# Kernel optimization log

Measured on AMD Instinct MI355X. Metric: run time of the kernel, lower is better.

The kernel has to match this reference:

```python
import jax, jax.numpy as jnp
import numpy as np

N, E = 50000, 800000
HID, HEADS, EDIM = 64, 4, 32
HC = HID * HEADS
NEG_SLOPE = 0.2
LN_EPS = 1e-5


def setup_inputs() -> dict:
    key = jax.random.key(0)
    ks = jax.random.split(key, 16)
    s = lambda d: 1.0 / np.sqrt(d)
    return {
        "x": jax.random.normal(ks[0], (N, HID), jnp.float32),
        "edge_index": jax.random.randint(ks[1], (2, E), 0, N, jnp.int64),
        "edge_attr": jax.random.normal(ks[2], (E, EDIM), jnp.float32),
        # GATv2Conv params
        "W_l": jax.random.normal(ks[3], (HID, HC), jnp.float32) * s(HID),
        "b_l": jnp.zeros((HC,), jnp.float32),
        "W_r": jax.random.normal(ks[4], (HID, HC), jnp.float32) * s(HID),
        "b_r": jnp.zeros((HC,), jnp.float32),
        "W_e": jax.random.normal(ks[5], (EDIM, HC), jnp.float32) * s(EDIM),
        "att": jax.random.normal(ks[6], (HEADS, HID), jnp.float32) * s(HID),
        "bias_gat": jnp.zeros((HC,), jnp.float32),
        # block params
        "W1": jax.random.normal(ks[7], (HID, HC), jnp.float32) * s(HID),
        "b1": jnp.zeros((HC,), jnp.float32),
        "gamma": jnp.ones((HC,), jnp.float32),
        "beta": jnp.zeros((HC,), jnp.float32),
        "W2": jax.random.normal(ks[8], (HC, HID), jnp.float32) * s(HC),
        "b2": jnp.zeros((HID,), jnp.float32),
    }


def _gatv2(x, edge_index, edge_attr, W_l, b_l, W_r, b_r, W_e, att, bias_gat):
    src, dst = edge_index[0], edge_index[1]
    x_l = (x @ W_l + b_l).reshape(N, HEADS, HID)  # source transform
    x_r = (x @ W_r + b_r).reshape(N, HEADS, HID)  # target transform
    e = (edge_attr @ W_e).reshape(E, HEADS, HID)
    m = x_l[src] + x_r[dst] + e                    # [E, H, C]
    m = jax.nn.leaky_relu(m, NEG_SLOPE)
    alpha = jnp.einsum('ehc,hc->eh', m, att)       # [E, H]
    # segment softmax over incoming edges of each target node
    amax = jax.ops.segment_max(alpha, dst, num_segments=N)
    alpha = jnp.exp(alpha - amax[dst])
    denom = jax.ops.segment_sum(alpha, dst, num_segments=N)
    alpha = alpha / (denom[dst] + 1e-16)
    out = jax.ops.segment_sum(x_l[src] * alpha[..., None], dst, num_segments=N)
    return out.reshape(N, HC) + bias_gat


def reference(x, edge_index, edge_attr, W_l, b_l, W_r, b_r, W_e, att, bias_gat,
              W1, b1, gamma, beta, W2, b2):
    h = _gatv2(x, edge_index, edge_attr, W_l, b_l, W_r, b_r, W_e, att, bias_gat)
    xl = jnp.tanh(x @ W1 + b1)
    z = xl + h
    mu = jnp.mean(z, axis=-1, keepdims=True)
    var = jnp.var(z, axis=-1, keepdims=True)
    z = (z - mu) * jax.lax.rsqrt(var + LN_EPS) * gamma + beta
    return jnp.tanh(z @ W2 + b2)
```

## Files before the change

kernel.cpp:

```cpp
#include <hip/hip_runtime.h>
#include <math.h>

#define N_NODES 50000
#define N_EDGES 800000
#define HID 64
#define HEADS 4
#define HC 256
#define NEG_SLOPE 0.2f
#define LN_EPS 1e-5f
#define EDGE_BLOCKS 2048

typedef __attribute__((ext_vector_type(8))) short bf16x8;
typedef __attribute__((ext_vector_type(8))) unsigned short u16x8;
typedef __attribute__((ext_vector_type(4))) float f32x4;

__device__ __forceinline__ float bf2f(unsigned short u) {
    return __uint_as_float(((unsigned int)u) << 16);
}
__device__ __forceinline__ unsigned short f2bf(float f) {
    unsigned int u = __float_as_uint(f);
    u = (u + 0x7fffu + ((u >> 16) & 1u)) >> 16;
    return (unsigned short)u;
}
__device__ __forceinline__ float fast_tanh(float v) {
    const float c = fminf(fmaxf(v, -15.f), 15.f);
    const float e = __expf(2.f * c);
    return 1.f - 2.f / (e + 1.f);
}
__device__ __forceinline__ bf16x8 pack_bf8(float4 a, float4 b) {
    u16x8 r;
    r[0] = f2bf(a.x); r[1] = f2bf(a.y); r[2] = f2bf(a.z); r[3] = f2bf(a.w);
    r[4] = f2bf(b.x); r[5] = f2bf(b.y); r[6] = f2bf(b.z); r[7] = f2bf(b.w);
    return __builtin_bit_cast(bf16x8, r);
}

__global__ __launch_bounds__(256) void k_ntm(
    const float* __restrict__ x,
    const float* __restrict__ W_l, const float* __restrict__ b_l,
    const float* __restrict__ W_r, const float* __restrict__ b_r,
    unsigned short* __restrict__ xl_t, unsigned short* __restrict__ xr_t)
{
    __shared__ unsigned short wl_s[2][16][64][8];
    __shared__ unsigned short wr_s[2][16][64][8];
    const int t = threadIdx.x, lane = t & 63, wv = t >> 6;
    const int arow = lane & 15, koct = lane >> 4;

    for (int i = t; i < 2048; i += 256) {
        const int ks = i >> 10, nt = (i >> 6) & 15, ls = i & 63;
        const int col = nt * 16 + (ls & 15);
        const int kb = ks * 32 + (ls >> 4) * 8;
        unsigned short a[8], b[8];
#pragma unroll
        for (int j = 0; j < 8; j++) {
            a[j] = f2bf(W_l[(kb + j) * 256 + col]);
            b[j] = f2bf(W_r[(kb + j) * 256 + col]);
        }
        *(ushort4*)&wl_s[ks][nt][ls][0] = make_ushort4(a[0], a[1], a[2], a[3]);
        *(ushort4*)&wl_s[ks][nt][ls][4] = make_ushort4(a[4], a[5], a[6], a[7]);
        *(ushort4*)&wr_s[ks][nt][ls][0] = make_ushort4(b[0], b[1], b[2], b[3]);
        *(ushort4*)&wr_s[ks][nt][ls][4] = make_ushort4(b[4], b[5], b[6], b[7]);
    }
    __syncthreads();

    const int n0w = blockIdx.x * 64 + wv * 16;
    if (n0w >= N_NODES) return;

    const float* xrow = x + (size_t)(n0w + arow) * 64;
    const bf16x8 af0 = pack_bf8(*(const float4*)(xrow + koct * 8),
                                *(const float4*)(xrow + koct * 8 + 4));
    const bf16x8 af1 = pack_bf8(*(const float4*)(xrow + 32 + koct * 8),
                                *(const float4*)(xrow + 32 + koct * 8 + 4));

    float acc[4][16];
#pragma unroll
    for (int nt = 0; nt < 16; nt++) {
        const float bv = b_l[nt * 16 + arow];
        f32x4 d = {bv, bv, bv, bv};
        d = __builtin_amdgcn_mfma_f32_16x16x32_bf16(af0, *(const bf16x8*)&wl_s[0][nt][lane][0], d, 0, 0, 0);
        d = __builtin_amdgcn_mfma_f32_16x16x32_bf16(af1, *(const bf16x8*)&wl_s[1][nt][lane][0], d, 0, 0, 0);
#pragma unroll
        for (int r = 0; r < 4; r++) acc[r][nt] = d[r];
    }
#pragma unroll
    for (int r = 0; r < 4; r++) {
        u16x8 lo, hi;
#pragma unroll
        for (int j = 0; j < 8; j++) { lo[j] = f2bf(acc[r][j]); hi[j] = f2bf(acc[r][j + 8]); }
        unsigned short* dst = xl_t + (size_t)(n0w + koct * 4 + r) * 256 + arow * 16;
        *(u16x8*)dst = lo;
        *(u16x8*)(dst + 8) = hi;
    }
#pragma unroll
    for (int nt = 0; nt < 16; nt++) {
        const float bv = b_r[nt * 16 + arow];
        f32x4 d = {bv, bv, bv, bv};
        d = __builtin_amdgcn_mfma_f32_16x16x32_bf16(af0, *(const bf16x8*)&wr_s[0][nt][lane][0], d, 0, 0, 0);
        d = __builtin_amdgcn_mfma_f32_16x16x32_bf16(af1, *(const bf16x8*)&wr_s[1][nt][lane][0], d, 0, 0, 0);
#pragma unroll
        for (int r = 0; r < 4; r++) acc[r][nt] = d[r];
    }
#pragma unroll
    for (int r = 0; r < 4; r++) {
        u16x8 lo, hi;
#pragma unroll
        for (int j = 0; j < 8; j++) { lo[j] = f2bf(acc[r][j]); hi[j] = f2bf(acc[r][j + 8]); }
        unsigned short* dst = xr_t + (size_t)(n0w + koct * 4 + r) * 256 + arow * 16;
        *(u16x8*)dst = lo;
        *(u16x8*)(dst + 8) = hi;
    }
}

__global__ __launch_bounds__(256) void k_permw(
    const float* __restrict__ W1, const float* __restrict__ b1,
    const float* __restrict__ gamma, const float* __restrict__ beta,
    const float* __restrict__ bias_gat, const float* __restrict__ W2,
    float* __restrict__ W1p, float* __restrict__ b1p,
    float* __restrict__ gammap, float* __restrict__ betap,
    float* __restrict__ biasgp, float* __restrict__ W2p)
{
    const int c = threadIdx.x;
    const int pos = (c & 15) * 16 + (c >> 4);
    for (int k = 0; k < 64; k++) W1p[k * 256 + pos] = W1[k * 256 + c];
    b1p[pos] = b1[c];
    gammap[pos] = gamma[c];
    betap[pos] = beta[c];
    biasgp[pos] = bias_gat[c];
    for (int j = 0; j < 64; j++) W2p[pos * 64 + j] = W2[c * 64 + j];
}

__global__ __launch_bounds__(256) void k_hist(const int* __restrict__ ei, int* __restrict__ count)
{
    const int e = blockIdx.x * 256 + threadIdx.x;
    if (e < N_EDGES) atomicAdd(&count[ei[N_EDGES + e]], 1);
}

__global__ __launch_bounds__(1024) void k_scan(const int* __restrict__ count, int* __restrict__ off)
{
    __shared__ int wsum[16];
    __shared__ int s_carry;
    const int t = threadIdx.x, lane = t & 63, wv = t >> 6;
    if (t == 0) s_carry = 0;
    __syncthreads();
    for (int base = 0; base < N_NODES; base += 8192) {
        const int idx0 = base + t * 8;
        int v[8];
#pragma unroll
        for (int j = 0; j < 8; j++) { int i = idx0 + j; v[j] = (i < N_NODES) ? count[i] : 0; }
#pragma unroll
        for (int j = 1; j < 8; j++) v[j] += v[j - 1];
        const int tot = v[7];
        int sc = tot;
#pragma unroll
        for (int s = 1; s < 64; s <<= 1) { int o = __shfl_up(sc, s, 64); if (lane >= s) sc += o; }
        if (lane == 63) wsum[wv] = sc;
        __syncthreads();
        const int carry = s_carry;
        int woff = 0;
        for (int u = 0; u < wv; u++) woff += wsum[u];
        const int ebase = carry + woff + (sc - tot);
#pragma unroll
        for (int j = 0; j < 8; j++) {
            int i = idx0 + j;
            if (i < N_NODES) off[i] = ebase + (j ? v[j - 1] : 0);
        }
        __syncthreads();
        if (t == 0) { int tt = 0; for (int u = 0; u < 16; u++) tt += wsum[u]; s_carry = carry + tt; }
        __syncthreads();
    }
    if (threadIdx.x == 0) off[N_NODES] = s_carry;
}

__global__ __launch_bounds__(256) void k_scatter(
    const int* __restrict__ ei, const int* __restrict__ off, int* __restrict__ cursor,
    int* __restrict__ csr_src, int* __restrict__ eid_csr)
{
    const int e = blockIdx.x * 256 + threadIdx.x;
    if (e < N_EDGES) {
        const int s = ei[e];
        const int d = ei[N_EDGES + e];
        const int pos = off[d] + atomicAdd(&cursor[d], 1);
        csr_src[pos] = s;
        eid_csr[pos] = e;
    }
}

template<bool F32>
__global__ __launch_bounds__(256) void k_edgeagg(
    const int* __restrict__ off, const int* __restrict__ csr_src,
    const int* __restrict__ eid_csr, const float* __restrict__ edge_attr,
    const float* __restrict__ W_e, const float* __restrict__ att,
    const unsigned short* __restrict__ xl_t, const unsigned short* __restrict__ xr_t,
    void* __restrict__ zs_g)
{
    __shared__ unsigned short bfrag_s[16][64][8];

    const int t = threadIdx.x;
    const int lane = t & 63, wv = t >> 6;
    const int arow = lane & 15, koct = lane >> 4;

    for (int i = t; i < 1024; i += 256) {
        const int nt = i >> 6, ls = i & 63;
        const int col = nt * 16 + (ls & 15);
        const int kb = (ls >> 4) * 8;
        unsigned short tmp[8];
#pragma unroll
        for (int j = 0; j < 8; j++) tmp[j] = f2bf(W_e[(kb + j) * 256 + col]);
        *(ushort4*)&bfrag_s[nt][ls][0] = make_ushort4(tmp[0], tmp[1], tmp[2], tmp[3]);
        *(ushort4*)&bfrag_s[nt][ls][4] = make_ushort4(tmp[4], tmp[5], tmp[6], tmp[7]);
    }
    __syncthreads();

    float attLf[8], attHf[8];
#pragma unroll
    for (int j = 0; j < 8; j++) {
        attLf[j] = att[j * 16 + arow];
        attHf[j] = att[(j + 8) * 16 + arow];
    }

    const int STRIDE = EDGE_BLOCKS * 4;
    int node = blockIdx.x * 4 + wv;
    if (node >= N_NODES) return;

    int lo = off[node], hi = off[node + 1];
    u16x8 xrl = *(const u16x8*)(xr_t + (size_t)node * 256 + arow * 16);
    u16x8 xrh = *(const u16x8*)(xr_t + (size_t)node * 256 + arow * 16 + 8);
    while (hi <= lo) {
        if (F32) *(float4*)((float*)zs_g + (size_t)node * 256 + arow * 16 + koct * 4) = make_float4(0.f, 0.f, 0.f, 0.f);
        else *(ushort4*)((unsigned short*)zs_g + (size_t)node * 256 + arow * 16 + koct * 4) = make_ushort4(0, 0, 0, 0);
        node += STRIDE;
        if (node >= N_NODES) return;
        lo = off[node]; hi = off[node + 1];
        xrl = *(const u16x8*)(xr_t + (size_t)node * 256 + arow * 16);
        xrh = *(const u16x8*)(xr_t + (size_t)node * 256 + arow * 16 + 8);
    }
    int svbase = lo;
    int svall = csr_src[min(svbase + lane, hi - 1)];
    int evall = eid_csr[min(svbase + lane, hi - 1)];

    int nnode = node + STRIDE;
    bool nvalid = nnode < N_NODES;
    int nlo = 0, nhi = 0, nsvall = 0, nevall = 0;
    u16x8 nxrl = xrl, nxrh = xrh;
    if (nvalid) {
        nlo = off[nnode]; nhi = off[nnode + 1];
        nxrl = *(const u16x8*)(xr_t + (size_t)nnode * 256 + arow * 16);
        nxrh = *(const u16x8*)(xr_t + (size_t)nnode * 256 + arow * 16 + 8);
        if (nhi > nlo) {
            nsvall = csr_src[min(nlo + lane, nhi - 1)];
            nevall = eid_csr[min(nlo + lane, nhi - 1)];
        }
    }
    int p0 = lo;
    bf16x8 af;
    u16x8 xlo[4], xhi[4];
    {
        const int eid0 = __shfl(evall, arow, 64);
        const float* ap = edge_attr + (size_t)eid0 * 32 + koct * 8;
        af = pack_bf8(*(const float4*)ap, *(const float4*)(ap + 4));
#pragma unroll
        for (int r = 0; r < 4; r++) {
            const int sr = __shfl(svall, koct * 4 + r, 64);
            const unsigned short* bp = xl_t + (size_t)sr * 256 + arow * 16;
            xlo[r] = *(const u16x8*)bp;
            xhi[r] = *(const u16x8*)(bp + 8);
        }
    }

    float g[16];
#pragma unroll
    for (int i = 0; i < 16; i++) g[i] = 0.f;
    float dsum[4] = {0.f, 0.f, 0.f, 0.f};

    for (;;) {
        const bool last = (p0 + 16 >= hi);
        bool uvalid;
        int up0;
        if (!last) { uvalid = true; up0 = p0 + 16; }
        else {
            while (nvalid && nlo >= nhi) {
                if (F32) *(float4*)((float*)zs_g + (size_t)nnode * 256 + arow * 16 + koct * 4) = make_float4(0.f, 0.f, 0.f, 0.f);
                else *(ushort4*)((unsigned short*)zs_g + (size_t)nnode * 256 + arow * 16 + koct * 4) = make_ushort4(0, 0, 0, 0);
                nnode += STRIDE;
                nvalid = nnode < N_NODES;
                if (nvalid) {
                    nlo = off[nnode]; nhi = off[nnode + 1];
                    nxrl = *(const u16x8*)(xr_t + (size_t)nnode * 256 + arow * 16);
                    nxrh = *(const u16x8*)(xr_t + (size_t)nnode * 256 + arow * 16 + 8);
                    if (nhi > nlo) {
                        nsvall = csr_src[min(nlo + lane, nhi - 1)];
                        nevall = eid_csr[min(nlo + lane, nhi - 1)];
                    }
                }
            }
            uvalid = nvalid; up0 = nlo;
        }
        float4 uA0 = make_float4(0.f, 0.f, 0.f, 0.f), uA1 = uA0;
        if (uvalid) {
            const int ubase = last ? 0 : (up0 - svbase);
            const int uev = last ? nevall : evall;
            const int ueid = __shfl(uev, ubase + arow, 64);
            const float* ap = edge_attr + (size_t)ueid * 32 + koct * 8;
            uA0 = *(const float4*)ap;
            uA1 = *(const float4*)(ap + 4);
        }

        float s_[4][4];
#pragma unroll
        for (int r = 0; r < 4; r++)
#pragma unroll
            for (int h = 0; h < 4; h++) s_[r][h] = 0.f;

#pragma unroll
        for (int nt = 0; nt < 8; nt++) {
            const bf16x8 bfr = *(const bf16x8*)&bfrag_s[nt][lane][0];
            const float xrv = bf2f((unsigned short)xrl[nt]);
            f32x4 dacc = {xrv, xrv, xrv, xrv};
            dacc = __builtin_amdgcn_mfma_f32_16x16x32_bf16(af, bfr, dacc, 0, 0, 0);
            const float atv = attLf[nt];
            const int h = nt >> 2;
#pragma unroll
            for (int r = 0; r < 4; r++) {
                const float mm = dacc[r] + bf2f((unsigned short)xlo[r][nt]);
                const float lk = fmaxf(mm, NEG_SLOPE * mm);
                s_[r][h] = fmaf(atv, lk, s_[r][h]);
            }
        }
        u16x8 uxlo[4], uxhi[4];
        if (uvalid) {
            const int ubase = last ? 0 : (up0 - svbase);
            const int usrcv = last ? nsvall : svall;
#pragma unroll
            for (int r = 0; r < 4; r++) {
                const int sr = __shfl(usrcv, ubase + koct * 4 + r, 64);
                const unsigned short* bp = xl_t + (size_t)sr * 256 + arow * 16;
                uxlo[r] = *(const u16x8*)bp;
                uxhi[r] = *(const u16x8*)(bp + 8);
            }
        } else {
#pragma unroll
            for (int r = 0; r < 4; r++) { uxlo[r] = xlo[r]; uxhi[r] = xhi[r]; }
        }
#pragma unroll
        for (int n2 = 0; n2 < 8; n2++) {
            const int nt = n2 + 8;
            const bf16x8 bfr = *(const bf16x8*)&bfrag_s[nt][lane][0];
            const float xrv = bf2f((unsigned short)xrh[n2]);
            f32x4 dacc = {xrv, xrv, xrv, xrv};
            dacc = __builtin_amdgcn_mfma_f32_16x16x32_bf16(af, bfr, dacc, 0, 0, 0);
            const float atv = attHf[n2];
            const int h = nt >> 2;
#pragma unroll
            for (int r = 0; r < 4; r++) {
                const float mm = dacc[r] + bf2f((unsigned short)xhi[r][n2]);
                const float lk = fmaxf(mm, NEG_SLOPE * mm);
                s_[r][h] = fmaf(atv, lk, s_[r][h]);
            }
        }
#pragma unroll
        for (int r = 0; r < 4; r++)
#pragma unroll
            for (int h = 0; h < 4; h++) {
                float v = s_[r][h];
                v += __shfl_xor(v, 1, 64);
                v += __shfl_xor(v, 2, 64);
                v += __shfl_xor(v, 4, 64);
                v += __shfl_xor(v, 8, 64);
                s_[r][h] = v;
            }
#pragma unroll
        for (int h = 0; h < 4; h++) {
            float w4[4];
#pragma unroll
            for (int r = 0; r < 4; r++) {
                const bool ok = (p0 + koct * 4 + r) < hi;
                w4[r] = ok ? __expf(fminf(s_[r][h], 60.f)) : 0.f;
            }
            dsum[h] += (w4[0] + w4[1]) + (w4[2] + w4[3]);
#pragma unroll
            for (int q = 0; q < 4; q++) {
                const int nt = h * 4 + q;
                float acc = g[nt];
#pragma unroll
                for (int r = 0; r < 4; r++) {
                    const float xv = bf2f((unsigned short)(nt < 8 ? xlo[r][nt & 7] : xhi[r][nt & 7]));
                    acc = fmaf(w4[r], xv, acc);
                }
                g[nt] = acc;
            }
        }

        if (last) {
#pragma unroll
            for (int i = 0; i < 16; i++) {
                float v = g[i];
                v += __shfl_xor(v, 16, 64);
                v += __shfl_xor(v, 32, 64);
                g[i] = v;
            }
#pragma unroll
            for (int h = 0; h < 4; h++) {
                float v = dsum[h];
                v += __shfl_xor(v, 16, 64);
                v += __shfl_xor(v, 32, 64);
                dsum[h] = v;
            }
            const float inv = 1.f / (dsum[koct] + 1e-16f);
            if (F32) {
                *(float4*)((float*)zs_g + (size_t)node * 256 + arow * 16 + koct * 4) =
                    make_float4(g[koct * 4] * inv, g[koct * 4 + 1] * inv,
                                g[koct * 4 + 2] * inv, g[koct * 4 + 3] * inv);
            } else {
                *(ushort4*)((unsigned short*)zs_g + (size_t)node * 256 + arow * 16 + koct * 4) =
                    make_ushort4(f2bf(g[koct * 4] * inv), f2bf(g[koct * 4 + 1] * inv),
                                 f2bf(g[koct * 4 + 2] * inv), f2bf(g[koct * 4 + 3] * inv));
            }
            if (!uvalid) return;
            node = nnode; lo = nlo; hi = nhi; xrl = nxrl; xrh = nxrh;
            svbase = nlo; svall = nsvall; evall = nevall;
#pragma unroll
            for (int i = 0; i < 16; i++) g[i] = 0.f;
#pragma unroll
            for (int h = 0; h < 4; h++) dsum[h] = 0.f;
            nnode += STRIDE;
            nvalid = nnode < N_NODES;
            if (nvalid) {
                nlo = off[nnode]; nhi = off[nnode + 1];
                nxrl = *(const u16x8*)(xr_t + (size_t)nnode * 256 + arow * 16);
                nxrh = *(const u16x8*)(xr_t + (size_t)nnode * 256 + arow * 16 + 8);
                if (nhi > nlo) {
                    nsvall = csr_src[min(nlo + lane, nhi - 1)];
                    nevall = eid_csr[min(nlo + lane, nhi - 1)];
                }
            }
        }
        p0 = up0;
        af = pack_bf8(uA0, uA1);
#pragma unroll
        for (int r = 0; r < 4; r++) { xlo[r] = uxlo[r]; xhi[r] = uxhi[r]; }
        if (p0 - svbase >= 32) {
            svbase = p0;
            svall = csr_src[min(svbase + lane, hi - 1)];
            evall = eid_csr[min(svbase + lane, hi - 1)];
        }
    }
}

template<bool F32>
__global__ __launch_bounds__(256) void k_post(
    const void* __restrict__ zs_g, const float* __restrict__ x,
    const float* __restrict__ biasgp,
    const float* __restrict__ W1p, const float* __restrict__ b1p,
    const float* __restrict__ gammap, const float* __restrict__ betap,
    const float* __restrict__ W2p, const float* __restrict__ b2,
    float* __restrict__ out)
{
    __shared__ unsigned short wf[16384];
    __shared__ unsigned short zsh[64][272];
    __shared__ float outsh[64][64];

    const int t = threadIdx.x, lane = t & 63, wv = t >> 6;
    const int arow = lane & 15, koct = lane >> 4;
    const int n0 = blockIdx.x * 64;
    const int nw = n0 + wv * 16;

    for (int i = t; i < 2048; i += 256) {
        const int ks = i >> 10, nt = (i >> 6) & 15, ls = i & 63;
        const int col = (ls & 15) * 16 + nt;
        const int kb = ks * 32 + (ls >> 4) * 8;
        unsigned short a[8];
#pragma unroll
        for (int j = 0; j < 8; j++) a[j] = f2bf(W1p[(kb + j) * 256 + col]);
        *(ushort4*)&wf[i * 8]     = make_ushort4(a[0], a[1], a[2], a[3]);
        *(ushort4*)&wf[i * 8 + 4] = make_ushort4(a[4], a[5], a[6], a[7]);
    }
    __syncthreads();

    const int xn = min(nw + arow, N_NODES - 1);
    const float* xrow = x + (size_t)xn * 64;
    const bf16x8 af0 = pack_bf8(*(const float4*)(xrow + koct * 8),
                                *(const float4*)(xrow + koct * 8 + 4));
    const bf16x8 af1 = pack_bf8(*(const float4*)(xrow + 32 + koct * 8),
                                *(const float4*)(xrow + 32 + koct * 8 + 4));

    float z[4][16];
#pragma unroll
    for (int nt = 0; nt < 16; nt++) {
        const float bv = b1p[arow * 16 + nt];
        f32x4 d = {bv, bv, bv, bv};
        d = __builtin_amdgcn_mfma_f32_16x16x32_bf16(af0, *(const bf16x8*)&wf[(0 * 16 + nt) * 512 + lane * 8], d, 0, 0, 0);
        d = __builtin_amdgcn_mfma_f32_16x16x32_bf16(af1, *(const bf16x8*)&wf[(1 * 16 + nt) * 512 + lane * 8], d, 0, 0, 0);
#pragma unroll
        for (int r = 0; r < 4; r++) z[r][nt] = d[r];
    }
#pragma unroll
    for (int r = 0; r < 4; r++) {
        const int nd = min(nw + koct * 4 + r, N_NODES - 1);
        float gv[16];
        if (F32) {
            const float* gp = (const float*)zs_g + (size_t)nd * 256 + arow * 16;
#pragma unroll
            for (int i4 = 0; i4 < 4; i4++) {
                const float4 v = *(const float4*)(gp + i4 * 4);
                gv[i4 * 4] = v.x; gv[i4 * 4 + 1] = v.y; gv[i4 * 4 + 2] = v.z; gv[i4 * 4 + 3] = v.w;
            }
        } else {
            const unsigned short* gp = (const unsigned short*)zs_g + (size_t)nd * 256 + arow * 16;
            const u16x8 a = *(const u16x8*)gp;
            const u16x8 b = *(const u16x8*)(gp + 8);
#pragma unroll
            for (int j = 0; j < 8; j++) { gv[j] = bf2f((unsigned short)a[j]); gv[j + 8] = bf2f((unsigned short)b[j]); }
        }
#pragma unroll
        for (int nt = 0; nt < 16; nt++)
            z[r][nt] = fast_tanh(z[r][nt]) + gv[nt] + biasgp[arow * 16 + nt];
    }
#pragma unroll
    for (int r = 0; r < 4; r++) {
        float s = 0.f, q = 0.f;
#pragma unroll
        for (int nt = 0; nt < 16; nt++) { s += z[r][nt]; q = fmaf(z[r][nt], z[r][nt], q); }
        s += __shfl_xor(s, 1, 64); q += __shfl_xor(q, 1, 64);
        s += __shfl_xor(s, 2, 64); q += __shfl_xor(q, 2, 64);
        s += __shfl_xor(s, 4, 64); q += __shfl_xor(q, 4, 64);
        s += __shfl_xor(s, 8, 64); q += __shfl_xor(q, 8, 64);
        const float mu = s * (1.f / 256.f);
        const float var = q * (1.f / 256.f) - mu * mu;
        const float ivn = rsqrtf(var + LN_EPS);
        u16x8 lo, hi;
#pragma unroll
        for (int nt = 0; nt < 16; nt++) {
            const float zn = (z[r][nt] - mu) * ivn * gammap[arow * 16 + nt] + betap[arow * 16 + nt];
            if (nt < 8) lo[nt] = f2bf(zn); else hi[nt - 8] = f2bf(zn);
        }
        unsigned short* dst = &zsh[wv * 16 + koct * 4 + r][arow * 16];
        *(u16x8*)dst = lo;
        *(u16x8*)(dst + 8) = hi;
    }
    __syncthreads();
    for (int i = t; i < 2048; i += 256) {
        const int kb = i >> 8, ct = (i >> 6) & 3, ls = i & 63;
        const int col = ct * 16 + (ls & 15);
        const int k0 = kb * 32 + (ls >> 4) * 8;
        unsigned short a[8];
#pragma unroll
        for (int j = 0; j < 8; j++) a[j] = f2bf(W2p[(k0 + j) * 64 + col]);
        *(ushort4*)&wf[i * 8]     = make_ushort4(a[0], a[1], a[2], a[3]);
        *(ushort4*)&wf[i * 8 + 4] = make_ushort4(a[4], a[5], a[6], a[7]);
    }
    __syncthreads();
    f32x4 acc2[4];
#pragma unroll
    for (int ct = 0; ct < 4; ct++) {
        const float bv = b2[ct * 16 + arow];
        acc2[ct][0] = bv; acc2[ct][1] = bv; acc2[ct][2] = bv; acc2[ct][3] = bv;
    }
#pragma unroll
    for (int kb = 0; kb < 8; kb++) {
        const bf16x8 a = *(const bf16x8*)&zsh[wv * 16 + arow][kb * 32 + koct * 8];
#pragma unroll
        for (int ct = 0; ct < 4; ct++)
            acc2[ct] = __builtin_amdgcn_mfma_f32_16x16x32_bf16(
                a, *(const bf16x8*)&wf[((kb * 4 + ct) * 64 + lane) * 8], acc2[ct], 0, 0, 0);
    }
#pragma unroll
    for (int ct = 0; ct < 4; ct++)
#pragma unroll
        for (int r = 0; r < 4; r++)
            outsh[wv * 16 + koct * 4 + r][ct * 16 + arow] = fast_tanh(acc2[ct][r]);
    __syncthreads();
    for (int i = t; i < 4096; i += 256) {
        const int row = i >> 6;
        if (n0 + row < N_NODES)
            out[(size_t)(n0 + row) * 64 + (i & 63)] = outsh[row][i & 63];
    }
}

extern "C" void kernel_launch(void* const* d_in, const int* in_sizes, int n_in,
                              void* d_out, int out_size, void* d_ws, size_t ws_size,
                              hipStream_t stream)
{
    const float* x         = (const float*)d_in[0];
    const int*   ei        = (const int*)d_in[1];
    const float* edge_attr = (const float*)d_in[2];
    const float* W_l       = (const float*)d_in[3];
    const float* b_l       = (const float*)d_in[4];
    const float* W_r       = (const float*)d_in[5];
    const float* b_r       = (const float*)d_in[6];
    const float* W_e       = (const float*)d_in[7];
    const float* att       = (const float*)d_in[8];
    const float* bias_gat  = (const float*)d_in[9];
    const float* W1        = (const float*)d_in[10];
    const float* b1        = (const float*)d_in[11];
    const float* gamma     = (const float*)d_in[12];
    const float* beta      = (const float*)d_in[13];
    const float* W2        = (const float*)d_in[14];
    const float* b2        = (const float*)d_in[15];
    float* out = (float*)d_out;

    char* wsb = (char*)d_ws;
    size_t o = 0;
    unsigned short* xl_t   = (unsigned short*)(wsb + o);  o += (size_t)N_NODES * HC * 2;
    unsigned short* xr_t   = (unsigned short*)(wsb + o);  o += (size_t)N_NODES * HC * 2;
    int* csr_src           = (int*)(wsb + o);             o += (size_t)N_EDGES * 4;
    int* eid_csr           = (int*)(wsb + o);             o += (size_t)N_EDGES * 4;
    int* count             = (int*)(wsb + o);             o += (size_t)N_NODES * 4;
    int* cursor            = (int*)(wsb + o);             o += (size_t)N_NODES * 4;
    int* off               = (int*)(wsb + o);             o += (size_t)(N_NODES + 1) * 4;
    float* W1p             = (float*)(wsb + o);           o += 64 * 256 * 4;
    float* W2p             = (float*)(wsb + o);           o += 256 * 64 * 4;
    float* b1p             = (float*)(wsb + o);           o += 256 * 4;
    float* gammap          = (float*)(wsb + o);           o += 256 * 4;
    float* betap           = (float*)(wsb + o);           o += 256 * 4;
    float* biasgp          = (float*)(wsb + o);           o += 256 * 4;
    o = (o + 255) & ~(size_t)255;
    void* zs_g             = (void*)(wsb + o);
    const bool f32ok = (o + (size_t)N_NODES * HC * 4) <= ws_size;

    hipMemsetAsync(count, 0, 2 * (size_t)N_NODES * sizeof(int), stream);

    k_ntm<<<(N_NODES + 63) / 64, 256, 0, stream>>>(x, W_l, b_l, W_r, b_r, xl_t, xr_t);
    k_permw<<<1, 256, 0, stream>>>(W1, b1, gamma, beta, bias_gat, W2,
                                   W1p, b1p, gammap, betap, biasgp, W2p);
    k_hist<<<(N_EDGES + 255) / 256, 256, 0, stream>>>(ei, count);
    k_scan<<<1, 1024, 0, stream>>>(count, off);
    k_scatter<<<(N_EDGES + 255) / 256, 256, 0, stream>>>(ei, off, cursor, csr_src, eid_csr);
    if (f32ok) {
        k_edgeagg<true><<<EDGE_BLOCKS, 256, 0, stream>>>(off, csr_src, eid_csr, edge_attr,
                                                         W_e, att, xl_t, xr_t, zs_g);
        k_post<true><<<(N_NODES + 63) / 64, 256, 0, stream>>>(zs_g, x, biasgp,
                                                              W1p, b1p, gammap, betap, W2p, b2, out);
    } else {
        k_edgeagg<false><<<EDGE_BLOCKS, 256, 0, stream>>>(off, csr_src, eid_csr, edge_attr,
                                                          W_e, att, xl_t, xr_t, zs_g);
        k_post<false><<<(N_NODES + 63) / 64, 256, 0, stream>>>(zs_g, x, biasgp,
                                                               W1p, b1p, gammap, betap, W2p, b2, out);
    }
}
```

Measured before the change: 528.3 us.

## Fuse histogram, weight permutation and edge_attr bf16 conversion into node transform kernel

Merges the degree histogram and the W1/W2 permutation kernels into the node-transform kernel, launched with a fixed grid of 783 blocks so each block also covers a slice of edges. The same kernel now pre-converts edge_attr to bf16 into workspace when space allows. The edge aggregation kernel then reads half-width bf16 edge features in its random gathers instead of fp32. This saves launches and gather bandwidth, at the cost of an extra full pass that reads fp32 edge_attr and writes the bf16 copy, plus more work per block in the node kernel.

```diff
diff --git a/kernel.cpp b/kernel.cpp
--- a/kernel.cpp
+++ b/kernel.cpp
@@ -9,6 +9,7 @@
 #define NEG_SLOPE 0.2f
 #define LN_EPS 1e-5f
 #define EDGE_BLOCKS 2048
+#define NTM_BLOCKS 783
 
 typedef __attribute__((ext_vector_type(8))) short bf16x8;
 typedef __attribute__((ext_vector_type(8))) unsigned short u16x8;
@@ -38,12 +39,54 @@
     const float* __restrict__ x,
     const float* __restrict__ W_l, const float* __restrict__ b_l,
     const float* __restrict__ W_r, const float* __restrict__ b_r,
+    const int* __restrict__ ei, int* __restrict__ count,
+    const float* __restrict__ edge_attr, unsigned short* __restrict__ ea_bf,
+    const int do_ea,
+    const float* __restrict__ W1, const float* __restrict__ b1,
+    const float* __restrict__ gamma, const float* __restrict__ beta,
+    const float* __restrict__ bias_gat, const float* __restrict__ W2,
+    float* __restrict__ W1p, float* __restrict__ b1p,
+    float* __restrict__ gammap, float* __restrict__ betap,
+    float* __restrict__ biasgp, float* __restrict__ W2p,
     unsigned short* __restrict__ xl_t, unsigned short* __restrict__ xr_t)
 {
     __shared__ unsigned short wl_s[2][16][64][8];
     __shared__ unsigned short wr_s[2][16][64][8];
     const int t = threadIdx.x, lane = t & 63, wv = t >> 6;
     const int arow = lane & 15, koct = lane >> 4;
+    const int bid = blockIdx.x;
+
+    {
+        const int e0 = bid * 1022;
+#pragma unroll
+        for (int j = 0; j < 4; j++) {
+            const int e = e0 + j * 256 + t;
+            if (e < e0 + 1022 && e < N_EDGES) atomicAdd(&count[ei[N_EDGES + e]], 1);
+        }
+    }
+    if (do_ea) {
+        const long long i0 = (long long)bid * 1022 * 8;
+        const long long iend = i0 + 1022 * 8;
+        const long long itot = (long long)N_EDGES * 8;
+        for (int j = 0; j < 32; j++) {
+            const long long idx = i0 + (long long)j * 256 + t;
+            if (idx < iend && idx < itot) {
+                const float4 v = *(const float4*)(edge_attr + idx * 4);
+                *(ushort4*)(ea_bf + idx * 4) =
+                    make_ushort4(f2bf(v.x), f2bf(v.y), f2bf(v.z), f2bf(v.w));
+            }
+        }
+    }
+    if (bid == NTM_BLOCKS - 1) {
+        const int c = t;
+        const int pos = (c & 15) * 16 + (c >> 4);
+        for (int k = 0; k < 64; k++) W1p[k * 256 + pos] = W1[k * 256 + c];
+        b1p[pos] = b1[c];
+        gammap[pos] = gamma[c];
+        betap[pos] = beta[c];
+        biasgp[pos] = bias_gat[c];
+        for (int j = 0; j < 64; j++) W2p[pos * 64 + j] = W2[c * 64 + j];
+    }
 
     for (int i = t; i < 2048; i += 256) {
         const int ks = i >> 10, nt = (i >> 6) & 15, ls = i & 63;
@@ -62,7 +105,7 @@
     }
     __syncthreads();
 
-    const int n0w = blockIdx.x * 64 + wv * 16;
+    const int n0w = bid * 64 + wv * 16;
     if (n0w >= N_NODES) return;
 
     const float* xrow = x + (size_t)(n0w + arow) * 64;
@@ -108,30 +151,6 @@
         *(u16x8*)dst = lo;
         *(u16x8*)(dst + 8) = hi;
     }
-}
-
-__global__ __launch_bounds__(256) void k_permw(
-    const float* __restrict__ W1, const float* __restrict__ b1,
-    const float* __restrict__ gamma, const float* __restrict__ beta,
-    const float* __restrict__ bias_gat, const float* __restrict__ W2,
-    float* __restrict__ W1p, float* __restrict__ b1p,
-    float* __restrict__ gammap, float* __restrict__ betap,
-    float* __restrict__ biasgp, float* __restrict__ W2p)
-{
-    const int c = threadIdx.x;
-    const int pos = (c & 15) * 16 + (c >> 4);
-    for (int k = 0; k < 64; k++) W1p[k * 256 + pos] = W1[k * 256 + c];
-    b1p[pos] = b1[c];
-    gammap[pos] = gamma[c];
-    betap[pos] = beta[c];
-    biasgp[pos] = bias_gat[c];
-    for (int j = 0; j < 64; j++) W2p[pos * 64 + j] = W2[c * 64 + j];
-}
-
-__global__ __launch_bounds__(256) void k_hist(const int* __restrict__ ei, int* __restrict__ count)
-{
-    const int e = blockIdx.x * 256 + threadIdx.x;
-    if (e < N_EDGES) atomicAdd(&count[ei[N_EDGES + e]], 1);
 }
 
 __global__ __launch_bounds__(1024) void k_scan(const int* __restrict__ count, int* __restrict__ off)
@@ -184,10 +203,11 @@
     }
 }
 
-template<bool F32>
+template<bool F32, bool EABF>
 __global__ __launch_bounds__(256) void k_edgeagg(
     const int* __restrict__ off, const int* __restrict__ csr_src,
     const int* __restrict__ eid_csr, const float* __restrict__ edge_attr,
+    const unsigned short* __restrict__ ea_bf,
     const float* __restrict__ W_e, const float* __restrict__ att,
     const unsigned short* __restrict__ xl_t, const unsigned short* __restrict__ xr_t,
     void* __restrict__ zs_g)
@@ -255,8 +275,12 @@
     u16x8 xlo[4], xhi[4];
     {
         const int eid0 = __shfl(evall, arow, 64);
-        const float* ap = edge_attr + (size_t)eid0 * 32 + koct * 8;
-        af = pack_bf8(*(const float4*)ap, *(const float4*)(ap + 4));
+        if (EABF) {
+            af = *(const bf16x8*)(ea_bf + (size_t)eid0 * 32 + koct * 8);
+        } else {
+            const float* ap = edge_attr + (size_t)eid0 * 32 + koct * 8;
+            af = pack_bf8(*(const float4*)ap, *(const float4*)(ap + 4));
+        }
 #pragma unroll
         for (int r = 0; r < 4; r++) {
             const int sr = __shfl(svall, koct * 4 + r, 64);
@@ -294,14 +318,19 @@
             }
             uvalid = nvalid; up0 = nlo;
         }
+        u16x8 uAb = {0, 0, 0, 0, 0, 0, 0, 0};
         float4 uA0 = make_float4(0.f, 0.f, 0.f, 0.f), uA1 = uA0;
         if (uvalid) {
             const int ubase = last ? 0 : (up0 - svbase);
             const int uev = last ? nevall : evall;
             const int ueid = __shfl(uev, ubase + arow, 64);
-            const float* ap = edge_attr + (size_t)ueid * 32 + koct * 8;
-            uA0 = *(const float4*)ap;
-            uA1 = *(const float4*)(ap + 4);
+            if (EABF) {
+                uAb = *(const u16x8*)(ea_bf + (size_t)ueid * 32 + koct * 8);
+            } else {
+                const float* ap = edge_attr + (size_t)ueid * 32 + koct * 8;
+                uA0 = *(const float4*)ap;
+                uA1 = *(const float4*)(ap + 4);
+            }
         }
 
         float s_[4][4];
@@ -434,7 +463,8 @@
             }
         }
         p0 = up0;
-        af = pack_bf8(uA0, uA1);
+        if (EABF) af = __builtin_bit_cast(bf16x8, uAb);
+        else af = pack_bf8(uA0, uA1);
 #pragma unroll
         for (int r = 0; r < 4; r++) { xlo[r] = uxlo[r]; xhi[r] = uxhi[r]; }
         if (p0 - svbase >= 32) {
@@ -614,24 +644,36 @@
     float* biasgp          = (float*)(wsb + o);           o += 256 * 4;
     o = (o + 255) & ~(size_t)255;
     void* zs_g             = (void*)(wsb + o);
-    const bool f32ok = (o + (size_t)N_NODES * HC * 4) <= ws_size;
+    const size_t zs_f32_bytes = (size_t)N_NODES * HC * 4;
+    const size_t ea_bytes     = (size_t)N_EDGES * 32 * 2;
+    const bool f32ok = (o + zs_f32_bytes) <= ws_size;
+    size_t o_ea = o + (f32ok ? zs_f32_bytes : (size_t)N_NODES * HC * 2);
+    o_ea = (o_ea + 255) & ~(size_t)255;
+    const bool eaok = (o_ea + ea_bytes) <= ws_size;
+    unsigned short* ea_bf = (unsigned short*)(wsb + o_ea);
 
     hipMemsetAsync(count, 0, 2 * (size_t)N_NODES * sizeof(int), stream);
 
-    k_ntm<<<(N_NODES + 63) / 64, 256, 0, stream>>>(x, W_l, b_l, W_r, b_r, xl_t, xr_t);
-    k_permw<<<1, 256, 0, stream>>>(W1, b1, gamma, beta, bias_gat, W2,
-                                   W1p, b1p, gammap, betap, biasgp, W2p);
-    k_hist<<<(N_EDGES + 255) / 256, 256, 0, stream>>>(ei, count);
+    k_ntm<<<NTM_BLOCKS, 256, 0, stream>>>(x, W_l, b_l, W_r, b_r,
+                                          ei, count, edge_attr, ea_bf, eaok ? 1 : 0,
+                                          W1, b1, gamma, beta, bias_gat, W2,
+                                          W1p, b1p, gammap, betap, biasgp, W2p,
+                                          xl_t, xr_t);
     k_scan<<<1, 1024, 0, stream>>>(count, off);
     k_scatter<<<(N_EDGES + 255) / 256, 256, 0, stream>>>(ei, off, cursor, csr_src, eid_csr);
-    if (f32ok) {
-        k_edgeagg<true><<<EDGE_BLOCKS, 256, 0, stream>>>(off, csr_src, eid_csr, edge_attr,
-                                                         W_e, att, xl_t, xr_t, zs_g);
+    if (f32ok && eaok) {
+        k_edgeagg<true, true><<<EDGE_BLOCKS, 256, 0, stream>>>(off, csr_src, eid_csr, edge_attr,
+                                                               ea_bf, W_e, att, xl_t, xr_t, zs_g);
+        k_post<true><<<(N_NODES + 63) / 64, 256, 0, stream>>>(zs_g, x, biasgp,
+                                                              W1p, b1p, gammap, betap, W2p, b2, out);
+    } else if (f32ok) {
+        k_edgeagg<true, false><<<EDGE_BLOCKS, 256, 0, stream>>>(off, csr_src, eid_csr, edge_attr,
+                                                                ea_bf, W_e, att, xl_t, xr_t, zs_g);
         k_post<true><<<(N_NODES + 63) / 64, 256, 0, stream>>>(zs_g, x, biasgp,
                                                               W1p, b1p, gammap, betap, W2p, b2, out);
     } else {
-        k_edgeagg<false><<<EDGE_BLOCKS, 256, 0, stream>>>(off, csr_src, eid_csr, edge_attr,
-                                                          W_e, att, xl_t, xr_t, zs_g);
+        k_edgeagg<false, false><<<EDGE_BLOCKS, 256, 0, stream>>>(off, csr_src, eid_csr, edge_attr,
+                                                                 ea_bf, W_e, att, xl_t, xr_t, zs_g);
         k_post<false><<<(N_NODES + 63) / 64, 256, 0, stream>>>(zs_g, x, biasgp,
                                                                W1p, b1p, gammap, betap, W2p, b2, out);
     }
```

After: 541.9 us. 1.03x slower.
